# Performance work log

Measured on AMD Instinct MI355X. Metric: run time of the kernel, lower is better.

The kernel has to match this reference:

```python
import jax, jax.numpy as jnp
import numpy as np

EPS = 1e-08

def _masked_stats(x, m, denom):
    # x: [B,C,H,W] already multiplied by mask; m: [B,1,H,W]; denom: [B,1,1,1]
    mean = jnp.sum(x, axis=(2, 3), keepdims=True) / denom          # [B,C,1,1]
    var = jnp.sum(((x - mean) * m) ** 2, axis=(2, 3), keepdims=True) / denom
    return mean, jnp.maximum(var, 0.0)

def _modulate(w, a, b):
    # concat [B,C,1,1]+[B,C,1,1] -> [B,2C], linear (no bias), back to [B,C,1,1]
    v = jnp.concatenate([a, b], axis=1)[:, :, 0, 0]                # [B,2C]
    y = v @ w.T                                                    # [B,C]
    return y[:, :, None, None]

def setup_inputs() -> dict:
    key = jax.random.key(0)
    ks = jax.random.split(key, 7)
    B, C, H, W = 4, 128, 256, 256
    x1 = jax.random.normal(ks[0], (B, C, H, W), dtype=jnp.float32)
    x2 = jax.random.normal(ks[1], (B, C, H, W), dtype=jnp.float32)
    mask = jax.random.uniform(ks[2], (B, 1, H // 2, W // 2), dtype=jnp.float32)
    w_in_mean = jax.random.normal(ks[3], (C, 2 * C), dtype=jnp.float32) * 0.05
    w_in_var = jax.random.normal(ks[4], (C, 2 * C), dtype=jnp.float32) * 0.05
    w_out_mean = jax.random.normal(ks[5], (C, 2 * C), dtype=jnp.float32) * 0.05
    w_out_var = jax.random.normal(ks[6], (C, 2 * C), dtype=jnp.float32) * 0.05
    return {"x1": x1, "x2": x2, "mask": mask,
            "w_in_mean": w_in_mean, "w_in_var": w_in_var,
            "w_out_mean": w_out_mean, "w_out_var": w_out_var}

def reference(x1, x2, mask, w_in_mean, w_in_var, w_out_mean, w_out_var):
    H, W = x1.shape[2], x1.shape[3]
    # nearest-neighbor upsample of mask to x1 spatial size (integer factor)
    rh, rw = H // mask.shape[2], W // mask.shape[3]
    m = jnp.repeat(jnp.repeat(mask, rh, axis=2), rw, axis=3)       # [B,1,H,W]
    om = 1.0 - m
    n_in = jnp.sum(m, axis=(2, 3), keepdims=True) + EPS            # [B,1,1,1]
    n_out = jnp.sum(om, axis=(2, 3), keepdims=True) + EPS

    x1_in, x2_in = x1 * m, x2 * m
    x1_out, x2_out = x1 * om, x2 * om

    x1_in_mean, x1_in_var = _masked_stats(x1_in, m, n_in)
    x2_in_mean, x2_in_var = _masked_stats(x2_in, m, n_in)
    x1_out_mean, x1_out_var = _masked_stats(x1_out, om, n_out)
    x2_out_mean, x2_out_var = _masked_stats(x2_out, om, n_out)

    ada_in_mean = _modulate(w_in_mean, x1_in_mean, x2_in_mean)
    ada_in_var = _modulate(w_in_var, x1_in_var, x2_in_var)
    ada_out_mean = _modulate(w_out_mean, x1_out_mean, x2_out_mean)
    ada_out_var = _modulate(w_out_var, x1_out_var, x2_out_var)

    norm_in = (x1_in - x1_in_mean) * jax.lax.rsqrt(x1_in_var + EPS)
    norm_out = (x1_out - x1_out_mean) * jax.lax.rsqrt(x1_out_var + EPS)
    ada_x1_in = norm_in * ada_in_var + ada_in_mean
    ada_x1_out = norm_out * ada_out_var + ada_out_mean
    return ada_x1_in * m + ada_x1_out * om
```

## Files before the change

kernel.cpp:

```cpp
#include <hip/hip_runtime.h>

#define EPS 1e-8f

using f32x4 = __attribute__((ext_vector_type(4))) float;

__global__ __launch_bounds__(256) void k_stats(
    const float* __restrict__ x1,
    const float* __restrict__ x2,
    const float* __restrict__ mask,
    float* __restrict__ stats)
{
    int blk   = blockIdx.x;
    int chunk = blk & 3;
    int bc    = blk >> 2;
    int b     = bc >> 7;
    int tid   = threadIdx.x;

    const size_t poff = (size_t)bc * 65536 + (size_t)chunk * 16384;
    const float* xp1 = x1 + poff;
    const float* xp2 = x2 + poff;
    const float* mp  = mask + b * 16384;
    const int gi0 = chunk * 16384 + tid * 8;

    float a[12];
#pragma unroll
    for (int j = 0; j < 12; ++j) a[j] = 0.f;

    int off0 = tid * 8;
    f32x4 c1a = *(const f32x4*)(xp1 + off0);
    f32x4 c1b = *(const f32x4*)(xp1 + off0 + 4);
    f32x4 c2a = *(const f32x4*)(xp2 + off0);
    f32x4 c2b = *(const f32x4*)(xp2 + off0 + 4);
    int h0 = gi0 >> 8, w0 = gi0 & 255;
    f32x4 cm = *(const f32x4*)(mp + (h0 >> 1) * 128 + (w0 >> 1));

    for (int g = 0; g < 8; ++g) {
        f32x4 n1a, n1b, n2a, n2b, nm;
        if (g < 7) {
            int off = (g + 1) * 2048 + tid * 8;
            int gi  = gi0 + (g + 1) * 2048;
            int h = gi >> 8, w = gi & 255;
            n1a = *(const f32x4*)(xp1 + off);
            n1b = *(const f32x4*)(xp1 + off + 4);
            n2a = *(const f32x4*)(xp2 + off);
            n2b = *(const f32x4*)(xp2 + off + 4);
            nm  = *(const f32x4*)(mp + (h >> 1) * 128 + (w >> 1));
        }
#pragma unroll
        for (int j = 0; j < 8; ++j) {
            float m  = cm[j >> 1];
            float om = 1.f - m;
            float m2 = m * m, om2 = om * om;
            float f1 = (j < 4) ? c1a[j & 3] : c1b[j & 3];
            float f2 = (j < 4) ? c2a[j & 3] : c2b[j & 3];
            float p1 = f1 * m2,  p2 = f2 * m2;
            a[0] += f1 * m;  a[1] += p1 * m;  a[2] += p1 * p1;
            a[3] += f2 * m;  a[4] += p2 * m;  a[5] += p2 * p2;
            float q1 = f1 * om2, q2 = f2 * om2;
            a[6] += f1 * om; a[7] += q1 * om; a[8] += q1 * q1;
            a[9] += f2 * om; a[10]+= q2 * om; a[11]+= q2 * q2;
        }
        c1a = n1a; c1b = n1b; c2a = n2a; c2b = n2b; cm = nm;
    }

#pragma unroll
    for (int j = 0; j < 12; ++j)
#pragma unroll
        for (int d = 32; d > 0; d >>= 1)
            a[j] += __shfl_down(a[j], d, 64);

    __shared__ float red[4][12];
    int wv = tid >> 6, ln = tid & 63;
    if (ln == 0) {
#pragma unroll
        for (int j = 0; j < 12; ++j) red[wv][j] = a[j];
    }
    __syncthreads();
    if (tid < 12) {
        float v = red[0][tid] + red[1][tid] + red[2][tid] + red[3][tid];
        stats[(size_t)blk * 12 + tid] = v;
    }
}

__global__ __launch_bounds__(256) void k_mod(
    const float* __restrict__ mask,
    const float* __restrict__ w_in_mean,
    const float* __restrict__ w_in_var,
    const float* __restrict__ w_out_mean,
    const float* __restrict__ w_out_var,
    const float* __restrict__ stats,
    float* __restrict__ derived)
{
    int b   = blockIdx.x >> 2;
    int mat = blockIdx.x & 3;
    int tid = threadIdx.x;

    const float* mp = mask + b * 16384;
    float sm = 0.f, sm2 = 0.f;
    for (int it = 0; it < 16; ++it) {
        const f32x4 mv = *(const f32x4*)(mp + (it * 256 + tid) * 4);
#pragma unroll
        for (int j = 0; j < 4; ++j) { float m = mv[j]; sm += m; sm2 += m * m; }
    }
#pragma unroll
    for (int d = 32; d > 0; d >>= 1) {
        sm  += __shfl_down(sm, d, 64);
        sm2 += __shfl_down(sm2, d, 64);
    }
    __shared__ float rr[8];
    __shared__ float SMs, SM2s;
    int wv = tid >> 6, ln = tid & 63;
    if (ln == 0) { rr[wv] = sm; rr[4 + wv] = sm2; }
    __syncthreads();
    if (tid == 0) {
        SMs  = 4.f * (rr[0] + rr[1] + rr[2] + rr[3]);
        SM2s = 4.f * (rr[4] + rr[5] + rr[6] + rr[7]);
    }
    __syncthreads();
    float SM = SMs, SM2 = SM2s;
    float n_in  = SM + EPS;
    float n_out = 65536.f - SM + EPS;
    float SOM2  = 65536.f - 2.f * SM + SM2;

    __shared__ float vec[256];

    if (tid < 128) {
        int c = tid;
        const float* st = stats + (size_t)(b * 128 + c) * 4 * 12;
        float s[12];
#pragma unroll
        for (int j = 0; j < 12; ++j)
            s[j] = (st[j] + st[12 + j]) + (st[24 + j] + st[36 + j]);
        float mi1 = s[0] / n_in;
        float vi1 = fmaxf((s[2] - 2.f * mi1 * s[1] + mi1 * mi1 * SM2) / n_in, 0.f);
        float mi2 = s[3] / n_in;
        float vi2 = fmaxf((s[5] - 2.f * mi2 * s[4] + mi2 * mi2 * SM2) / n_in, 0.f);
        float mo1 = s[6] / n_out;
        float vo1 = fmaxf((s[8] - 2.f * mo1 * s[7] + mo1 * mo1 * SOM2) / n_out, 0.f);
        float mo2 = s[9] / n_out;
        float vo2 = fmaxf((s[11] - 2.f * mo2 * s[10] + mo2 * mo2 * SOM2) / n_out, 0.f);
        float v0, v1;
        if (mat == 0)      { v0 = mi1; v1 = mi2; }
        else if (mat == 1) { v0 = vi1; v1 = vi2; }
        else if (mat == 2) { v0 = mo1; v1 = mo2; }
        else               { v0 = vo1; v1 = vo2; }
        vec[c] = v0; vec[128 + c] = v1;
        if (mat == 0) {
            float* d = derived + (size_t)(b * 128 + c) * 8;
            d[0] = mi1; d[1] = rsqrtf(vi1 + EPS);
            d[2] = mo1; d[3] = rsqrtf(vo1 + EPS);
        }
    }
    __syncthreads();

    const float* wp = (mat == 0) ? w_in_mean :
                      (mat == 1) ? w_in_var :
                      (mat == 2) ? w_out_mean : w_out_var;
    int row = tid >> 1, half = tid & 1;
    const float* wr = wp + row * 256 + half * 128;
    const float* vp = vec + half * 128;
    float acc = 0.f;
    for (int k = 0; k < 128; k += 4) {
        f32x4 w4 = *(const f32x4*)(wr + k);
#pragma unroll
        for (int j = 0; j < 4; ++j) acc += w4[j] * vp[k + j];
    }
    acc += __shfl_xor(acc, 1, 64);
    if (half == 0)
        derived[(size_t)(b * 128 + row) * 8 + 4 + mat] = acc;
}

__global__ __launch_bounds__(256) void k_apply(
    const float* __restrict__ x1,
    const float* __restrict__ mask,
    const float* __restrict__ derived,
    float* __restrict__ out)
{
    int blk   = blockIdx.x;
    int bc    = blk >> 2;
    int chunk = blk & 3;
    int b     = bc >> 7;
    const float* d = derived + (size_t)bc * 8;
    float mean_in = d[0], inv_in = d[1], mean_out = d[2], inv_out = d[3];
    float am_in = d[4], av_in = d[5], am_out = d[6], av_out = d[7];
    float ci1 = inv_in * av_in;
    float ci0 = am_in - mean_in * ci1;
    float co1 = inv_out * av_out;
    float co0 = am_out - mean_out * co1;

    int tid = threadIdx.x;
    const float* xp = x1 + (size_t)bc * 65536;
    float* op = out + (size_t)bc * 65536;
    const float* mp = mask + b * 16384;
    const int gi0 = chunk * 16384 + tid * 8;

    f32x4 cxa = *(const f32x4*)(xp + gi0);
    f32x4 cxb = *(const f32x4*)(xp + gi0 + 4);
    int h0 = gi0 >> 8, w0 = gi0 & 255;
    f32x4 cm = *(const f32x4*)(mp + (h0 >> 1) * 128 + (w0 >> 1));

    for (int g = 0; g < 8; ++g) {
        f32x4 nxa, nxb, nm;
        if (g < 7) {
            int gi = gi0 + (g + 1) * 2048;
            int h = gi >> 8, w = gi & 255;
            nxa = *(const f32x4*)(xp + gi);
            nxb = *(const f32x4*)(xp + gi + 4);
            nm  = *(const f32x4*)(mp + (h >> 1) * 128 + (w >> 1));
        }
        f32x4 oa, ob;
#pragma unroll
        for (int j = 0; j < 8; ++j) {
            float m  = cm[j >> 1];
            float om = 1.f - m;
            float x  = (j < 4) ? cxa[j & 3] : cxb[j & 3];
            float r  = x * (m * m * ci1 + om * om * co1) + ci0 * m + co0 * om;
            if (j < 4) oa[j & 3] = r; else ob[j & 3] = r;
        }
        int go = gi0 + g * 2048;
        __builtin_nontemporal_store(oa, (f32x4*)(op + go));
        __builtin_nontemporal_store(ob, (f32x4*)(op + go + 4));
        cxa = nxa; cxb = nxb; cm = nm;
    }
}

extern "C" void kernel_launch(void* const* d_in, const int* in_sizes, int n_in,
                              void* d_out, int out_size, void* d_ws, size_t ws_size,
                              hipStream_t stream) {
    const float* x1        = (const float*)d_in[0];
    const float* x2        = (const float*)d_in[1];
    const float* mask      = (const float*)d_in[2];
    const float* w_in_mean = (const float*)d_in[3];
    const float* w_in_var  = (const float*)d_in[4];
    const float* w_out_mean= (const float*)d_in[5];
    const float* w_out_var = (const float*)d_in[6];

    float* stats   = (float*)d_ws;
    float* derived = stats + 2048 * 12;
    float* out = (float*)d_out;

    k_stats<<<512 * 4, 256, 0, stream>>>(x1, x2, mask, stats);
    k_mod<<<4 * 4, 256, 0, stream>>>(mask, w_in_mean, w_in_var, w_out_mean, w_out_var,
                                     stats, derived);
    k_apply<<<512 * 4, 256, 0, stream>>>(x1, mask, derived, out);
}
```

Baseline: 361.5 us.

## Stage x1/x2 loads through LDS with async global_load_lds double buffering

Both the stats and apply kernels now copy input tiles into shared memory with direct global-to-LDS async loads, double-buffered across eight stages, and the compute reads from LDS. This is meant to keep more memory requests in flight and take register-staged prefetch off the vector registers. In exchange it adds a barrier per stage and an extra LDS round trip. The element-to-thread mapping and the mask indexing are rewritten to match the new layout.

After: 367.4 us. No clear change (+1.6%).

```diff
diff --git a/kernel.cpp b/kernel.cpp
--- a/kernel.cpp
+++ b/kernel.cpp
@@ -3,6 +3,10 @@
 #define EPS 1e-8f
 
 using f32x4 = __attribute__((ext_vector_type(4))) float;
+
+#define GLD16(g, l) __builtin_amdgcn_global_load_lds( \
+    (const __attribute__((address_space(1))) void*)(g), \
+    (__attribute__((address_space(3))) void*)(l), 16, 0, 0)
 
 __global__ __launch_bounds__(256) void k_stats(
     const float* __restrict__ x1,
@@ -10,58 +14,63 @@
     const float* __restrict__ mask,
     float* __restrict__ stats)
 {
+    __shared__ float lds[2][4096];
+
     int blk   = blockIdx.x;
     int chunk = blk & 3;
     int bc    = blk >> 2;
     int b     = bc >> 7;
     int tid   = threadIdx.x;
-
-    const size_t poff = (size_t)bc * 65536 + (size_t)chunk * 16384;
-    const float* xp1 = x1 + poff;
-    const float* xp2 = x2 + poff;
-    const float* mp  = mask + b * 16384;
-    const int gi0 = chunk * 16384 + tid * 8;
+    int wv    = tid >> 6, ln = tid & 63;
+
+    const size_t pbase = (size_t)bc * 65536 + (size_t)chunk * 16384
+                       + (size_t)(wv * 512 + ln * 8);
+    const float* sx1 = x1 + pbase;
+    const float* sx2 = x2 + pbase;
+    const float* mbase = mask + b * 16384 + (chunk * 32 + wv) * 128 + (ln & 31) * 4;
 
     float a[12];
 #pragma unroll
     for (int j = 0; j < 12; ++j) a[j] = 0.f;
 
-    int off0 = tid * 8;
-    f32x4 c1a = *(const f32x4*)(xp1 + off0);
-    f32x4 c1b = *(const f32x4*)(xp1 + off0 + 4);
-    f32x4 c2a = *(const f32x4*)(xp2 + off0);
-    f32x4 c2b = *(const f32x4*)(xp2 + off0 + 4);
-    int h0 = gi0 >> 8, w0 = gi0 & 255;
-    f32x4 cm = *(const f32x4*)(mp + (h0 >> 1) * 128 + (w0 >> 1));
-
-    for (int g = 0; g < 8; ++g) {
-        f32x4 n1a, n1b, n2a, n2b, nm;
-        if (g < 7) {
-            int off = (g + 1) * 2048 + tid * 8;
-            int gi  = gi0 + (g + 1) * 2048;
-            int h = gi >> 8, w = gi & 255;
-            n1a = *(const f32x4*)(xp1 + off);
-            n1b = *(const f32x4*)(xp1 + off + 4);
-            n2a = *(const f32x4*)(xp2 + off);
-            n2b = *(const f32x4*)(xp2 + off + 4);
-            nm  = *(const f32x4*)(mp + (h >> 1) * 128 + (w >> 1));
-        }
+#define KS_STAGE(D, S) { \
+      float* Lx1 = &lds[D][wv * 512]; \
+      float* Lx2 = &lds[D][2048 + wv * 512]; \
+      const float* g1 = sx1 + (S) * 2048; \
+      const float* g2 = sx2 + (S) * 2048; \
+      GLD16(g1, Lx1); GLD16(g1 + 4, Lx1 + 256); \
+      GLD16(g2, Lx2); GLD16(g2 + 4, Lx2 + 256); }
+
+    KS_STAGE(0, 0)
+    __syncthreads();
+
+    for (int s = 0; s < 8; ++s) {
+        int cur = s & 1;
+        if (s < 7) KS_STAGE(cur ^ 1, s + 1)
+        f32x4 mv = *(const f32x4*)(mbase + s * 512);
+        const float* LC1 = &lds[cur][wv * 512];
+        const float* LC2 = &lds[cur][2048 + wv * 512];
+        f32x4 v1a = *(const f32x4*)(LC1 + ln * 4);
+        f32x4 v1b = *(const f32x4*)(LC1 + 256 + ln * 4);
+        f32x4 v2a = *(const f32x4*)(LC2 + ln * 4);
+        f32x4 v2b = *(const f32x4*)(LC2 + 256 + ln * 4);
 #pragma unroll
         for (int j = 0; j < 8; ++j) {
-            float m  = cm[j >> 1];
+            float m  = mv[j >> 1];
             float om = 1.f - m;
             float m2 = m * m, om2 = om * om;
-            float f1 = (j < 4) ? c1a[j & 3] : c1b[j & 3];
-            float f2 = (j < 4) ? c2a[j & 3] : c2b[j & 3];
+            float f1 = (j < 4) ? v1a[j & 3] : v1b[j & 3];
+            float f2 = (j < 4) ? v2a[j & 3] : v2b[j & 3];
             float p1 = f1 * m2,  p2 = f2 * m2;
             a[0] += f1 * m;  a[1] += p1 * m;  a[2] += p1 * p1;
             a[3] += f2 * m;  a[4] += p2 * m;  a[5] += p2 * p2;
             float q1 = f1 * om2, q2 = f2 * om2;
-            a[6] += f1 * om; a[7] += q1 * om; a[8] += q1 * q1;
-            a[9] += f2 * om; a[10]+= q2 * om; a[11]+= q2 * q2;
+            a[6] += f1 * om; a[7]  += q1 * om; a[8]  += q1 * q1;
+            a[9] += f2 * om; a[10] += q2 * om; a[11] += q2 * q2;
         }
-        c1a = n1a; c1b = n1b; c2a = n2a; c2b = n2b; cm = nm;
-    }
+        __syncthreads();
+    }
+#undef KS_STAGE
 
 #pragma unroll
     for (int j = 0; j < 12; ++j)
@@ -69,15 +78,13 @@
         for (int d = 32; d > 0; d >>= 1)
             a[j] += __shfl_down(a[j], d, 64);
 
-    __shared__ float red[4][12];
-    int wv = tid >> 6, ln = tid & 63;
     if (ln == 0) {
 #pragma unroll
-        for (int j = 0; j < 12; ++j) red[wv][j] = a[j];
+        for (int j = 0; j < 12; ++j) lds[0][wv * 12 + j] = a[j];
     }
     __syncthreads();
     if (tid < 12) {
-        float v = red[0][tid] + red[1][tid] + red[2][tid] + red[3][tid];
+        float v = lds[0][tid] + lds[0][12 + tid] + lds[0][24 + tid] + lds[0][36 + tid];
         stats[(size_t)blk * 12 + tid] = v;
     }
 }
@@ -176,52 +183,57 @@
     const float* __restrict__ derived,
     float* __restrict__ out)
 {
+    __shared__ float lds[2][2048];
+
     int blk   = blockIdx.x;
     int bc    = blk >> 2;
     int chunk = blk & 3;
     int b     = bc >> 7;
-    const float* d = derived + (size_t)bc * 8;
-    float mean_in = d[0], inv_in = d[1], mean_out = d[2], inv_out = d[3];
-    float am_in = d[4], av_in = d[5], am_out = d[6], av_out = d[7];
-    float ci1 = inv_in * av_in;
-    float ci0 = am_in - mean_in * ci1;
-    float co1 = inv_out * av_out;
-    float co0 = am_out - mean_out * co1;
-
-    int tid = threadIdx.x;
-    const float* xp = x1 + (size_t)bc * 65536;
-    float* op = out + (size_t)bc * 65536;
-    const float* mp = mask + b * 16384;
-    const int gi0 = chunk * 16384 + tid * 8;
-
-    f32x4 cxa = *(const f32x4*)(xp + gi0);
-    f32x4 cxb = *(const f32x4*)(xp + gi0 + 4);
-    int h0 = gi0 >> 8, w0 = gi0 & 255;
-    f32x4 cm = *(const f32x4*)(mp + (h0 >> 1) * 128 + (w0 >> 1));
-
-    for (int g = 0; g < 8; ++g) {
-        f32x4 nxa, nxb, nm;
-        if (g < 7) {
-            int gi = gi0 + (g + 1) * 2048;
-            int h = gi >> 8, w = gi & 255;
-            nxa = *(const f32x4*)(xp + gi);
-            nxb = *(const f32x4*)(xp + gi + 4);
-            nm  = *(const f32x4*)(mp + (h >> 1) * 128 + (w >> 1));
-        }
+    int tid   = threadIdx.x;
+    int wv    = tid >> 6, ln = tid & 63;
+
+    f32x4 d0 = *(const f32x4*)(derived + (size_t)bc * 8);
+    f32x4 d1 = *(const f32x4*)(derived + (size_t)bc * 8 + 4);
+    float ci1 = d0[1] * d1[1];
+    float ci0 = d1[0] - d0[0] * ci1;
+    float co1 = d0[3] * d1[3];
+    float co0 = d1[2] - d0[2] * co1;
+
+    const size_t pbase = (size_t)bc * 65536 + (size_t)chunk * 16384
+                       + (size_t)(wv * 512 + ln * 8);
+    const float* sx = x1 + pbase;
+    float* op = out + pbase;
+    const float* mbase = mask + b * 16384 + (chunk * 32 + wv) * 128 + (ln & 31) * 4;
+
+#define KA_STAGE(D, S) { \
+      float* L = &lds[D][wv * 512]; \
+      const float* g = sx + (S) * 2048; \
+      GLD16(g, L); GLD16(g + 4, L + 256); }
+
+    KA_STAGE(0, 0)
+    __syncthreads();
+
+    for (int s = 0; s < 8; ++s) {
+        int cur = s & 1;
+        if (s < 7) KA_STAGE(cur ^ 1, s + 1)
+        f32x4 mv = *(const f32x4*)(mbase + s * 512);
+        const float* LC = &lds[cur][wv * 512];
+        f32x4 xa = *(const f32x4*)(LC + ln * 4);
+        f32x4 xb = *(const f32x4*)(LC + 256 + ln * 4);
         f32x4 oa, ob;
 #pragma unroll
         for (int j = 0; j < 8; ++j) {
-            float m  = cm[j >> 1];
+            float m  = mv[j >> 1];
             float om = 1.f - m;
-            float x  = (j < 4) ? cxa[j & 3] : cxb[j & 3];
+            float x  = (j < 4) ? xa[j & 3] : xb[j & 3];
             float r  = x * (m * m * ci1 + om * om * co1) + ci0 * m + co0 * om;
             if (j < 4) oa[j & 3] = r; else ob[j & 3] = r;
         }
-        int go = gi0 + g * 2048;
-        __builtin_nontemporal_store(oa, (f32x4*)(op + go));
-        __builtin_nontemporal_store(ob, (f32x4*)(op + go + 4));
-        cxa = nxa; cxb = nxb; cm = nm;
-    }
+        __builtin_nontemporal_store(oa, (f32x4*)(op + s * 2048));
+        __builtin_nontemporal_store(ob, (f32x4*)(op + s * 2048 + 4));
+        __syncthreads();
+    }
+#undef KA_STAGE
 }
 
 extern "C" void kernel_launch(void* const* d_in, const int* in_sizes, int n_in,
```
